# Kernel optimization log

Measured on AMD Instinct MI355X. Metric: run time of the kernel, lower is better.

Reference implementation:

```python
import jax, jax.numpy as jnp
import numpy as np

B, NV, NC, D, GD = 4, 2048, 8192, 64, 8


def setup_inputs() -> dict:
    key = jax.random.key(0)
    ks = jax.random.split(key, 16)
    f32 = jnp.float32
    rn = lambda k, s, fan: (jax.random.normal(k, s, dtype=f32) / np.float32(np.sqrt(fan)))
    raw = jax.random.randint(ks[0], (B, NC, NV), 0, 20)
    c_mat = jnp.where(raw == 0, -1.0, jnp.where(raw == 1, 1.0, 0.0)).astype(f32)
    v_mat = jnp.transpose(c_mat, (0, 2, 1))  # [B, NV, NC]
    variables = jax.random.normal(ks[1], (B, NV, D), dtype=f32)
    ground_vars = jax.random.normal(ks[2], (B, NV, GD), dtype=f32)
    # learned params
    c_block = rn(ks[3], (2, D, D), D)  # pos/neg literal projections (clause side)
    v_block = rn(ks[4], (2, D, D), D)  # pos/neg literal projections (variable side)
    vb = jax.random.normal(ks[5], (D,), dtype=f32)
    cb = jax.random.normal(ks[6], (D,), dtype=f32)
    Wg = rn(ks[7], (D, GD + D), GD + D)  # ground combiner Linear(concat) -> D
    bg = jnp.zeros((D,), f32)
    Wz = rn(ks[8], (D, D), D); Uz = rn(ks[9], (D, D), D); bz = jnp.zeros((D,), f32)
    Wr = rn(ks[10], (D, D), D); Ur = rn(ks[11], (D, D), D); br = jnp.zeros((D,), f32)
    Wh = rn(ks[12], (D, D), D); Uh = rn(ks[13], (D, D), D); bh = jnp.zeros((D,), f32)
    return dict(variables=variables, ground_vars=ground_vars, c_mat=c_mat, v_mat=v_mat,
                c_block=c_block, v_block=v_block, vb=vb, cb=cb, Wg=Wg, bg=bg,
                Wz=Wz, Uz=Uz, bz=bz, Wr=Wr, Ur=Ur, br=br, Wh=Wh, Uh=Uh, bh=bh)


def reference(variables, ground_vars, c_mat, v_mat, c_block, v_block, vb, cb,
              Wg, bg, Wz, Uz, bz, Wr, Ur, br, Wh, Uh, bh):
    b, nv, d = variables.shape
    v = variables.reshape(-1, d)  # [B*NV, D]
    # clause-side literal projections: bmm(c_block, v^T)^T == v @ c_block[i]^T
    pos_vars = (v @ c_block[0].T).reshape(b, nv, d)
    neg_vars = (v @ c_block[1].T).reshape(b, nv, d)
    pos_cmat = jnp.clip(c_mat, 0.0, 1.0)
    neg_cmat = -jnp.clip(c_mat, -1.0, 0.0)
    c = (jnp.einsum('bcv,bvd->bcd', pos_cmat, pos_vars)
         + jnp.einsum('bcv,bvd->bcd', neg_cmat, neg_vars))  # [B, NC, D]
    c = jax.nn.relu(c + cb)
    cv = c.reshape(-1, d)  # [B*NC, D]
    pos_cvars = (cv @ v_block[0].T).reshape(b, -1, d)
    neg_cvars = (cv @ v_block[1].T).reshape(b, -1, d)
    pos_vmat = jnp.clip(v_mat, 0.0, 1.0)
    neg_vmat = -jnp.clip(v_mat, -1.0, 0.0)
    nv_msg = (jnp.einsum('bvc,bcd->bvd', pos_vmat, pos_cvars)
              + jnp.einsum('bvc,bcd->bvd', neg_vmat, neg_cvars))  # [B, NV, D]
    v_emb = jax.nn.relu(nv_msg + vb).reshape(-1, d)
    # ground combiner: tanh(Linear(concat(ground, v_emb)))
    g = ground_vars.reshape(-1, ground_vars.shape[-1])
    av = jnp.tanh(jnp.concatenate([g, v_emb], axis=-1) @ Wg.T + bg)
    # GRU update against previous variable embeddings
    prev = v
    z = jax.nn.sigmoid(av @ Wz.T + prev @ Uz.T + bz)
    r = jax.nn.sigmoid(av @ Wr.T + prev @ Ur.T + br)
    h_tilda = jnp.tanh(av @ Wh.T + (r * prev) @ Uh.T + bh)
    h = (1.0 - z) * prev + z * h_tilda
    return h.reshape(b, nv * d, 1)
```

## Files before the change

### kernel.cpp

```cpp
#include <hip/hip_runtime.h>
#include <hip/hip_bf16.h>
#include <stdint.h>

#define NBATCH 4
#define NV 2048
#define NC 8192
#define DD 64

typedef __attribute__((ext_vector_type(8))) short s16x8;
typedef __attribute__((ext_vector_type(4))) float fx4;
typedef __attribute__((ext_vector_type(8))) unsigned short u16x8;
typedef __attribute__((ext_vector_type(4))) int i32x4;
typedef __attribute__((ext_vector_type(2))) unsigned int u32x2;

static __device__ __forceinline__ unsigned short bf16_rne(float x) {
    union { float f; unsigned int u; } v; v.f = x;
    unsigned int u = v.u;
    u += 0x7FFFu + ((u >> 16) & 1u);
    return (unsigned short)(u >> 16);
}
static __device__ __forceinline__ float bf16_f32(unsigned short h) {
    union { unsigned int u; float f; } v; v.u = ((unsigned int)h) << 16;
    return v.f;
}
static __device__ __forceinline__ void gload_lds16(const void* g, void* l) {
    __builtin_amdgcn_global_load_lds(
        (const __attribute__((address_space(1))) unsigned int*)g,
        (__attribute__((address_space(3))) unsigned int*)l, 16, 0, 0);
}

__global__ __launch_bounds__(256) void k_prep_pv(
    const float* __restrict__ vars, const float* __restrict__ cblk,
    char* __restrict__ qsh, char* __restrict__ qsl,
    char* __restrict__ qdh, char* __restrict__ qdl)
{
    __shared__ float sv[32][64];
    __shared__ float scb[2][64][65];
    int blk = blockIdx.x;
    int b = blk >> 6, ch = blk & 63;
    int t = threadIdx.x;
    const float* vsrc = vars + ((size_t)b * NV + (size_t)ch * 32) * DD;
    for (int i = t; i < 32 * 64; i += 256) sv[i >> 6][i & 63] = vsrc[i];
    for (int i = t; i < 2 * 64 * 64; i += 256) {
        int pn = i >> 12, dout = (i >> 6) & 63, k = i & 63;
        scb[pn][k][dout] = cblk[i];
    }
    __syncthreads();
    int ks = t >> 6, dout = t & 63;
    unsigned int wsh[2] = {0, 0}, wsl[2] = {0, 0}, wdh[2] = {0, 0}, wdl[2] = {0, 0};
    #pragma unroll
    for (int c8 = 0; c8 < 8; ++c8) {
        int vloc = ks * 8 + c8;
        float ap = 0.f, an = 0.f;
        for (int k = 0; k < 64; ++k) {
            float vv = sv[vloc][k];
            ap += vv * scb[0][k][dout];
            an += vv * scb[1][k][dout];
        }
        float s = (ap + an) * 0.5f, dv = (ap - an) * 0.5f;
        int qs_ = (int)rintf(s * 4096.f);
        int qd_ = (int)rintf(dv * 4096.f);
        qs_ = min(max(qs_, -32511), 32511);
        qd_ = min(max(qd_, -32511), 32511);
        int sh = (qs_ + 128) >> 8, sl = qs_ - (sh << 8);
        int dh = (qd_ + 128) >> 8, dl = qd_ - (dh << 8);
        int w = c8 >> 2, sft = (c8 & 3) * 8;
        wsh[w] |= (unsigned int)(sh & 0xFF) << sft;
        wsl[w] |= (unsigned int)(sl & 0xFF) << sft;
        wdh[w] |= (unsigned int)(dh & 0xFF) << sft;
        wdl[w] |= (unsigned int)(dl & 0xFF) << sft;
    }
    int kc = ch >> 1;
    int lg = ((ch & 1) << 1) | (ks >> 1);
    size_t off = (((size_t)(b * 32 + kc) * 64 + dout) * 4 + lg) * 16 + (ks & 1) * 8;
    *(u32x2*)(qsh + off) = (u32x2){wsh[0], wsh[1]};
    *(u32x2*)(qsl + off) = (u32x2){wsl[0], wsl[1]};
    *(u32x2*)(qdh + off) = (u32x2){wdh[0], wdh[1]};
    *(u32x2*)(qdl + off) = (u32x2){wdl[0], wdl[1]};
}

__global__ __launch_bounds__(512, 4) void k_phaseA(
    const float* __restrict__ cmat,
    const char* __restrict__ qsh, const char* __restrict__ qsl,
    const char* __restrict__ qdh, const char* __restrict__ qdl,
    const float* __restrict__ cb,
    float* __restrict__ cfull, unsigned short* __restrict__ comp)
{
    __shared__ char lds[2][16384];
    int blk = blockIdx.x;
    int b = blk & 3;
    int rg = blk >> 2;
    int t = threadIdx.x;
    int wv = t >> 6, l = t & 63, lr = l & 15, lg = l >> 4;
    int row0 = rg * 128 + wv * 16;
    const float* A0 = cmat + (size_t)b * NC * NV + (size_t)(row0 + lr) * NV + lg * 16;
    unsigned short* compb = comp + (size_t)b * 256 * NC;

    i32x4 ahi[4], alo[4];
    #pragma unroll
    for (int n = 0; n < 4; ++n) { ahi[n] = (i32x4){0,0,0,0}; alo[n] = (i32x4){0,0,0,0}; }

    if (t < 256) {
        size_t gb = ((size_t)(b * 32)) * 4096 + (size_t)t * 16;
        char* lp = &lds[0][t * 16];
        gload_lds16(qsh + gb, lp);
        gload_lds16(qsl + gb, lp + 4096);
        gload_lds16(qdh + gb, lp + 8192);
        gload_lds16(qdl + gb, lp + 12288);
    }
    fx4 xc[4], xn[4];
    #pragma unroll
    for (int j4 = 0; j4 < 4; ++j4) xc[j4] = *(const fx4*)(A0 + j4 * 4);
    __syncthreads();

    int cur = 0;
    #pragma unroll 1
    for (int kc = 0; kc < 32; ++kc) {
        if (kc < 31) {
            if (t < 256) {
                size_t gb = ((size_t)(b * 32 + kc + 1)) * 4096 + (size_t)t * 16;
                char* lp = &lds[cur ^ 1][t * 16];
                gload_lds16(qsh + gb, lp);
                gload_lds16(qsl + gb, lp + 4096);
                gload_lds16(qdh + gb, lp + 8192);
                gload_lds16(qdl + gb, lp + 12288);
            }
            #pragma unroll
            for (int j4 = 0; j4 < 4; ++j4)
                xn[j4] = *(const fx4*)(A0 + (kc + 1) * 64 + j4 * 4);
        }
        int tt[16];
        #pragma unroll
        for (int j = 0; j < 16; ++j) tt[j] = (int)xc[j >> 2][j & 3];
        i32x4 Asgn, Aabs;
        #pragma unroll
        for (int w = 0; w < 4; ++w)
            Asgn[w] = (unsigned int)(tt[4*w] & 0xFF) | ((unsigned int)(tt[4*w+1] & 0xFF) << 8)
                    | ((unsigned int)(tt[4*w+2] & 0xFF) << 16) | ((unsigned int)(tt[4*w+3] & 0xFF) << 24);
        #pragma unroll
        for (int w = 0; w < 4; ++w) Aabs[w] = Asgn[w] & 0x01010101;
        {
            unsigned int b0 = 0, b1 = 0;
            #pragma unroll
            for (int j = 0; j < 8; ++j) b0 |= ((unsigned int)tt[j] & 3u) << (2 * j);
            #pragma unroll
            for (int j = 0; j < 8; ++j) b1 |= ((unsigned int)tt[8 + j] & 3u) << (2 * j);
            int v8 = kc * 8 + lg * 2;
            int crow = row0 + lr;
            compb[(size_t)v8 * NC + crow] = (unsigned short)b0;
            compb[(size_t)(v8 + 1) * NC + crow] = (unsigned short)b1;
        }
        const char* bufp = lds[cur];
        #pragma unroll
        for (int n = 0; n < 4; ++n) {
            int boff = ((n * 16 + lr) * 4 + lg) * 16;
            i32x4 Bsh = *(const i32x4*)(bufp + boff);
            i32x4 Bsl = *(const i32x4*)(bufp + 4096 + boff);
            i32x4 Bdh = *(const i32x4*)(bufp + 8192 + boff);
            i32x4 Bdl = *(const i32x4*)(bufp + 12288 + boff);
            ahi[n] = __builtin_amdgcn_mfma_i32_16x16x64_i8(Aabs, Bsh, ahi[n], 0, 0, 0);
            ahi[n] = __builtin_amdgcn_mfma_i32_16x16x64_i8(Asgn, Bdh, ahi[n], 0, 0, 0);
            alo[n] = __builtin_amdgcn_mfma_i32_16x16x64_i8(Aabs, Bsl, alo[n], 0, 0, 0);
            alo[n] = __builtin_amdgcn_mfma_i32_16x16x64_i8(Asgn, Bdl, alo[n], 0, 0, 0);
        }
        if (kc < 31) {
            #pragma unroll
            for (int j4 = 0; j4 < 4; ++j4) xc[j4] = xn[j4];
        }
        __syncthreads();
        cur ^= 1;
    }
    float* dst = cfull + ((size_t)b * NC + row0) * DD;
    #pragma unroll
    for (int n = 0; n < 4; ++n) {
        int col = n * 16 + lr;
        float cbv = cb[col];
        #pragma unroll
        for (int r = 0; r < 4; ++r) {
            float v = (float)(ahi[n][r] * 256 + alo[n][r]) * (1.0f / 4096.0f) + cbv;
            dst[(size_t)(lg * 4 + r) * DD + col] = fmaxf(v, 0.f);
        }
    }
}

__global__ __launch_bounds__(256) void k_projC(
    const float* __restrict__ cfull,
    const float* __restrict__ vblk,
    unsigned short* __restrict__ csh, unsigned short* __restrict__ csl,
    unsigned short* __restrict__ cdh, unsigned short* __restrict__ cdl)
{
    __shared__ float src[32][64];
    __shared__ float svb[2][64][65];
    int blk = blockIdx.x;
    int b = blk >> 8, kc = blk & 255;
    int t = threadIdx.x;
    const float* cs = cfull + ((size_t)b * NC + (size_t)kc * 32) * DD;
    for (int i = t; i < 2048; i += 256) src[i >> 6][i & 63] = cs[i];
    for (int i = t; i < 8192; i += 256) {
        int pn = i >> 12, dout = (i >> 6) & 63, k = i & 63;
        svb[pn][k][dout] = vblk[i];
    }
    __syncthreads();
    int ks = t >> 6, dout = t & 63;
    float ap[8] = {0.f, 0.f, 0.f, 0.f, 0.f, 0.f, 0.f, 0.f};
    float an[8] = {0.f, 0.f, 0.f, 0.f, 0.f, 0.f, 0.f, 0.f};
    for (int k = 0; k < 64; ++k) {
        float w0 = svb[0][k][dout], w1 = svb[1][k][dout];
        #pragma unroll
        for (int c8 = 0; c8 < 8; ++c8) {
            float rc = src[ks * 8 + c8][k];
            ap[c8] += rc * w0;
            an[c8] += rc * w1;
        }
    }
    u16x8 vsh, vsl, vdh, vdl;
    #pragma unroll
    for (int c8 = 0; c8 < 8; ++c8) {
        float s = (ap[c8] + an[c8]) * 0.5f, dv = (ap[c8] - an[c8]) * 0.5f;
        unsigned short h = bf16_rne(s);
        vsh[c8] = h; vsl[c8] = bf16_rne(s - bf16_f32(h));
        h = bf16_rne(dv);
        vdh[c8] = h; vdl[c8] = bf16_rne(dv - bf16_f32(h));
    }
    size_t obase = (size_t)b * NC * DD + (((size_t)kc * 4 + ks) * 64 + dout) * 8;
    *(u16x8*)(csh + obase) = vsh;
    *(u16x8*)(csl + obase) = vsl;
    *(u16x8*)(cdh + obase) = vdh;
    *(u16x8*)(cdl + obase) = vdl;
}

__global__ __launch_bounds__(256, 2) void k_phaseB(
    const unsigned short* __restrict__ comp,
    const unsigned short* __restrict__ csh, const unsigned short* __restrict__ csl,
    const unsigned short* __restrict__ cdh, const unsigned short* __restrict__ cdl,
    float* __restrict__ npart)
{
    __shared__ short lds[2][16384];
    int blk = blockIdx.x;
    int combo = blk & 63;
    int rg = blk >> 6;
    int b = combo >> 4;
    int q = combo & 15;
    int t = threadIdx.x;
    int wv = t >> 6, l = t & 63, lr = l & 15, lg = l >> 4;
    int v0 = rg * 256 + wv * 64;
    const unsigned short* compb = comp + (size_t)b * 256 * NC;
    const size_t cvb = (size_t)b * NC * DD;
    int sh_ = 2 * (lr & 7);
    const unsigned short* cp[4];
    #pragma unroll
    for (int rt = 0; rt < 4; ++rt)
        cp[rt] = compb + (size_t)((v0 + rt * 16 + lr) >> 3) * NC + q * 512 + lg * 8;

    fx4 acc[4][4];
    #pragma unroll
    for (int i = 0; i < 4; ++i)
        #pragma unroll
        for (int j = 0; j < 4; ++j) acc[i][j] = (fx4){0.f, 0.f, 0.f, 0.f};

    {
        size_t gb = cvb + (size_t)(q * 8) * 4096 + (size_t)t * 8;
        short* lp = &lds[0][t * 8];
        gload_lds16(csh + gb, lp);           gload_lds16(csh + gb + 2048, lp + 2048);
        gload_lds16(csl + gb, lp + 4096);    gload_lds16(csl + gb + 2048, lp + 6144);
        gload_lds16(cdh + gb, lp + 8192);    gload_lds16(cdh + gb + 2048, lp + 10240);
        gload_lds16(cdl + gb, lp + 12288);   gload_lds16(cdl + gb + 2048, lp + 14336);
    }
    u16x8 uc[4][2], un[4][2];
    #pragma unroll
    for (int rt = 0; rt < 4; ++rt) {
        uc[rt][0] = *(const u16x8*)(cp[rt]);
        uc[rt][1] = *(const u16x8*)(cp[rt] + 32);
    }
    __syncthreads();

    int cur = 0;
    #pragma unroll 1
    for (int cc = 0; cc < 8; ++cc) {
        if (cc < 7) {
            size_t gb = cvb + (size_t)(q * 8 + cc + 1) * 4096 + (size_t)t * 8;
            short* lp = &lds[cur ^ 1][t * 8];
            gload_lds16(csh + gb, lp);           gload_lds16(csh + gb + 2048, lp + 2048);
            gload_lds16(csl + gb, lp + 4096);    gload_lds16(csl + gb + 2048, lp + 6144);
            gload_lds16(cdh + gb, lp + 8192);    gload_lds16(cdh + gb + 2048, lp + 10240);
            gload_lds16(cdl + gb, lp + 12288);   gload_lds16(cdl + gb + 2048, lp + 14336);
            #pragma unroll
            for (int rt = 0; rt < 4; ++rt) {
                un[rt][0] = *(const u16x8*)(cp[rt] + (cc + 1) * 64);
                un[rt][1] = *(const u16x8*)(cp[rt] + (cc + 1) * 64 + 32);
            }
        }
        const short* bufp = &lds[cur][0];
        #pragma unroll
        for (int st = 0; st < 2; ++st) {
            s16x8 As[4], Aa[4];
            #pragma unroll
            for (int rt = 0; rt < 4; ++rt) {
                #pragma unroll
                for (int i = 0; i < 8; ++i) {
                    unsigned int tb = ((unsigned int)uc[rt][st][i] >> sh_) & 3u;
                    unsigned short m = (tb & 1u) ? (unsigned short)0x3F80 : (unsigned short)0;
                    As[rt][i] = (short)m;
                    Aa[rt][i] = (short)(m | ((tb & 2u) << 14));
                }
            }
            #pragma unroll
            for (int n = 0; n < 4; ++n) {
                int off = ((st * 4 + lg) * 64 + n * 16 + lr) * 8;
                s16x8 Bs0 = *(const s16x8*)(bufp + off);
                s16x8 Bs1 = *(const s16x8*)(bufp + 4096 + off);
                s16x8 Bd0 = *(const s16x8*)(bufp + 8192 + off);
                s16x8 Bd1 = *(const s16x8*)(bufp + 12288 + off);
                #pragma unroll
                for (int rt = 0; rt < 4; ++rt) {
                    acc[rt][n] = __builtin_amdgcn_mfma_f32_16x16x32_bf16(As[rt], Bs0, acc[rt][n], 0, 0, 0);
                    acc[rt][n] = __builtin_amdgcn_mfma_f32_16x16x32_bf16(As[rt], Bs1, acc[rt][n], 0, 0, 0);
                    acc[rt][n] = __builtin_amdgcn_mfma_f32_16x16x32_bf16(Aa[rt], Bd0, acc[rt][n], 0, 0, 0);
                    acc[rt][n] = __builtin_amdgcn_mfma_f32_16x16x32_bf16(Aa[rt], Bd1, acc[rt][n], 0, 0, 0);
                }
            }
        }
        if (cc < 7) {
            #pragma unroll
            for (int rt = 0; rt < 4; ++rt) { uc[rt][0] = un[rt][0]; uc[rt][1] = un[rt][1]; }
        }
        __syncthreads();
        cur ^= 1;
    }
    float* dst = npart + (((size_t)q * NBATCH + b) * NV + v0) * DD;
    #pragma unroll
    for (int rt = 0; rt < 4; ++rt)
        #pragma unroll
        for (int n = 0; n < 4; ++n)
            #pragma unroll
            for (int r = 0; r < 4; ++r)
                dst[(size_t)(rt * 16 + lg * 4 + r) * DD + n * 16 + lr] = acc[rt][n][r];
}

__global__ __launch_bounds__(512) void k_gru(
    const float* __restrict__ npart, const float* __restrict__ vars,
    const float* __restrict__ gv, const float* __restrict__ vb,
    const float* __restrict__ Wg, const float* __restrict__ bg,
    const float* __restrict__ Wz, const float* __restrict__ Uz, const float* __restrict__ bz,
    const float* __restrict__ Wr, const float* __restrict__ Ur, const float* __restrict__ brr,
    const float* __restrict__ Wh, const float* __restrict__ Uh, const float* __restrict__ bh,
    float* __restrict__ out)
{
    __shared__ float sWg[72][65];
    __shared__ float sWz[64][65], sUz[64][65];
    __shared__ float sWr[64][65], sUr[64][65];
    __shared__ float sWh[64][65], sUh[64][65];
    __shared__ float scat[8][72];
    __shared__ float sprev[8][64];
    __shared__ float sav[8][64];
    __shared__ float srp[8][64];
    int t = threadIdx.x;
    for (int i = t * 4; i < 4608; i += 2048) {
        fx4 g4 = *(const fx4*)(Wg + i);
        int dout = i / 72, j = i - dout * 72;
        #pragma unroll
        for (int jj = 0; jj < 4; ++jj) sWg[j + jj][dout] = g4[jj];
    }
    for (int i = t * 4; i < 4096; i += 2048) {
        int dout = i >> 6, k = i & 63;
        fx4 a;
        a = *(const fx4*)(Wz + i);
        #pragma unroll
        for (int jj = 0; jj < 4; ++jj) sWz[k + jj][dout] = a[jj];
        a = *(const fx4*)(Uz + i);
        #pragma unroll
        for (int jj = 0; jj < 4; ++jj) sUz[k + jj][dout] = a[jj];
        a = *(const fx4*)(Wr + i);
        #pragma unroll
        for (int jj = 0; jj < 4; ++jj) sWr[k + jj][dout] = a[jj];
        a = *(const fx4*)(Ur + i);
        #pragma unroll
        for (int jj = 0; jj < 4; ++jj) sUr[k + jj][dout] = a[jj];
        a = *(const fx4*)(Wh + i);
        #pragma unroll
        for (int jj = 0; jj < 4; ++jj) sWh[k + jj][dout] = a[jj];
        a = *(const fx4*)(Uh + i);
        #pragma unroll
        for (int jj = 0; jj < 4; ++jj) sUh[k + jj][dout] = a[jj];
    }
    int rr = t >> 6, dout = t & 63;
    const size_t qs = (size_t)NBATCH * NV * DD;
    #pragma unroll 1
    for (int it = 0; it < 4; ++it) {
        size_t row = (size_t)blockIdx.x * 32 + it * 8 + rr;
        float prev = vars[row * 64 + dout];
        float ve = vb[dout];
        #pragma unroll
        for (int s = 0; s < 16; ++s) ve += npart[(size_t)s * qs + row * 64 + dout];
        ve = fmaxf(ve, 0.f);
        scat[rr][8 + dout] = ve;
        if (dout < 8) scat[rr][dout] = gv[row * 8 + dout];
        sprev[rr][dout] = prev;
        __syncthreads();
        float a = bg[dout];
        for (int j = 0; j < 72; ++j) a += scat[rr][j] * sWg[j][dout];
        float av = 1.f - 2.f / (__expf(2.f * a) + 1.f);
        sav[rr][dout] = av;
        __syncthreads();
        float zi = bz[dout], ri = brr[dout], hwa = 0.f;
        for (int k = 0; k < 64; ++k) {
            float ak = sav[rr][k], pk = sprev[rr][k];
            zi += ak * sWz[k][dout] + pk * sUz[k][dout];
            ri += ak * sWr[k][dout] + pk * sUr[k][dout];
            hwa += ak * sWh[k][dout];
        }
        float z = 1.f / (1.f + __expf(-zi));
        float rgate = 1.f / (1.f + __expf(-ri));
        srp[rr][dout] = rgate * prev;
        __syncthreads();
        float hin = bh[dout] + hwa;
        for (int k = 0; k < 64; ++k) hin += srp[rr][k] * sUh[k][dout];
        float ht = 1.f - 2.f / (__expf(2.f * hin) + 1.f);
        out[row * 64 + dout] = (1.f - z) * prev + z * ht;
        __syncthreads();
    }
}

extern "C" void kernel_launch(void* const* d_in, const int* in_sizes, int n_in,
                              void* d_out, int out_size, void* d_ws, size_t ws_size,
                              hipStream_t stream) {
    (void)in_sizes; (void)n_in; (void)out_size; (void)ws_size;
    const float* vars = (const float*)d_in[0];
    const float* gv   = (const float*)d_in[1];
    const float* cmat = (const float*)d_in[2];
    const float* cblk = (const float*)d_in[4];
    const float* vblk = (const float*)d_in[5];
    const float* vb   = (const float*)d_in[6];
    const float* cb   = (const float*)d_in[7];
    const float* Wg   = (const float*)d_in[8];
    const float* bg   = (const float*)d_in[9];
    const float* Wz   = (const float*)d_in[10];
    const float* Uz   = (const float*)d_in[11];
    const float* bz   = (const float*)d_in[12];
    const float* Wr   = (const float*)d_in[13];
    const float* Ur   = (const float*)d_in[14];
    const float* br_  = (const float*)d_in[15];
    const float* Wh   = (const float*)d_in[16];
    const float* Uh   = (const float*)d_in[17];
    const float* bh   = (const float*)d_in[18];
    float* out = (float*)d_out;

    char* w = (char*)d_ws;
    const size_t MB = 1024 * 1024;
    char* qsh = w + 0 * MB;
    char* qsl = w + 1 * MB;
    char* qdh = w + 2 * MB;
    char* qdl = w + 3 * MB;
    unsigned short* csh = (unsigned short*)(w + 4 * MB);
    unsigned short* csl = (unsigned short*)(w + 8 * MB);
    unsigned short* cdh = (unsigned short*)(w + 12 * MB);
    unsigned short* cdl = (unsigned short*)(w + 16 * MB);
    float* cfull         = (float*)(w + 20 * MB);
    float* npart         = (float*)(w + 28 * MB);
    unsigned short* comp = (unsigned short*)(w + 60 * MB);

    k_prep_pv<<<256, 256, 0, stream>>>(vars, cblk, qsh, qsl, qdh, qdl);
    k_phaseA<<<256, 512, 0, stream>>>(cmat, qsh, qsl, qdh, qdl, cb, cfull, comp);
    k_projC<<<1024, 256, 0, stream>>>(cfull, vblk, csh, csl, cdh, cdl);
    k_phaseB<<<512, 256, 0, stream>>>(comp, csh, csl, cdh, cdl, npart);
    k_gru<<<256, 512, 0, stream>>>(npart, vars, gv, vb, Wg, bg,
                                   Wz, Uz, bz, Wr, Ur, br_, Wh, Uh, bh, out);
}
```

Before: 175.5 us.

## Split phaseA/phaseB reductions across more blocks and drop LDS staging

Phase A now splits the variable dimension into two halves, with four times as many smaller blocks writing partial clause sums. Bias and ReLU move into k_projC, which adds the two partials. Phase B uses smaller 16-row tiles per wave with an 8-way split over clauses, and the GRU kernel runs more blocks over fewer rows each. Both matmul kernels drop double-buffered LDS staging and read B operands straight from global memory, relying on cache and higher occupancy for latency hiding. The trade-off is more partial-sum traffic and redundant B reads through L2.

```diff
diff --git a/kernel.cpp b/kernel.cpp
--- a/kernel.cpp
+++ b/kernel.cpp
@@ -22,11 +22,6 @@
 static __device__ __forceinline__ float bf16_f32(unsigned short h) {
     union { unsigned int u; float f; } v; v.u = ((unsigned int)h) << 16;
     return v.f;
-}
-static __device__ __forceinline__ void gload_lds16(const void* g, void* l) {
-    __builtin_amdgcn_global_load_lds(
-        (const __attribute__((address_space(1))) unsigned int*)g,
-        (__attribute__((address_space(3))) unsigned int*)l, 16, 0, 0);
 }
 
 __global__ __launch_bounds__(256) void k_prep_pv(
@@ -79,56 +74,37 @@
     *(u32x2*)(qdl + off) = (u32x2){wdl[0], wdl[1]};
 }
 
-__global__ __launch_bounds__(512, 4) void k_phaseA(
+__global__ __launch_bounds__(256, 4) void k_phaseA(
     const float* __restrict__ cmat,
     const char* __restrict__ qsh, const char* __restrict__ qsl,
     const char* __restrict__ qdh, const char* __restrict__ qdl,
-    const float* __restrict__ cb,
-    float* __restrict__ cfull, unsigned short* __restrict__ comp)
-{
-    __shared__ char lds[2][16384];
+    float* __restrict__ cpart, unsigned short* __restrict__ comp)
+{
     int blk = blockIdx.x;
-    int b = blk & 3;
-    int rg = blk >> 2;
+    int combo = blk & 7;
+    int rg = blk >> 3;
+    int b = combo >> 1;
+    int q = combo & 1;
     int t = threadIdx.x;
     int wv = t >> 6, l = t & 63, lr = l & 15, lg = l >> 4;
-    int row0 = rg * 128 + wv * 16;
-    const float* A0 = cmat + (size_t)b * NC * NV + (size_t)(row0 + lr) * NV + lg * 16;
+    int row = rg * 64 + wv * 16 + lr;
+    const float* A0 = cmat + (size_t)b * NC * NV + (size_t)row * NV + q * 1024 + lg * 16;
     unsigned short* compb = comp + (size_t)b * 256 * NC;
+    const char* qb0 = qsh + ((size_t)(b * 32 + q * 16)) * 4096;
+    const char* qb1 = qsl + ((size_t)(b * 32 + q * 16)) * 4096;
+    const char* qb2 = qdh + ((size_t)(b * 32 + q * 16)) * 4096;
+    const char* qb3 = qdl + ((size_t)(b * 32 + q * 16)) * 4096;
 
     i32x4 ahi[4], alo[4];
     #pragma unroll
     for (int n = 0; n < 4; ++n) { ahi[n] = (i32x4){0,0,0,0}; alo[n] = (i32x4){0,0,0,0}; }
 
-    if (t < 256) {
-        size_t gb = ((size_t)(b * 32)) * 4096 + (size_t)t * 16;
-        char* lp = &lds[0][t * 16];
-        gload_lds16(qsh + gb, lp);
-        gload_lds16(qsl + gb, lp + 4096);
-        gload_lds16(qdh + gb, lp + 8192);
-        gload_lds16(qdl + gb, lp + 12288);
-    }
-    fx4 xc[4], xn[4];
-    #pragma unroll
-    for (int j4 = 0; j4 < 4; ++j4) xc[j4] = *(const fx4*)(A0 + j4 * 4);
-    __syncthreads();
-
-    int cur = 0;
     #pragma unroll 1
-    for (int kc = 0; kc < 32; ++kc) {
-        if (kc < 31) {
-            if (t < 256) {
-                size_t gb = ((size_t)(b * 32 + kc + 1)) * 4096 + (size_t)t * 16;
-                char* lp = &lds[cur ^ 1][t * 16];
-                gload_lds16(qsh + gb, lp);
-                gload_lds16(qsl + gb, lp + 4096);
-                gload_lds16(qdh + gb, lp + 8192);
-                gload_lds16(qdl + gb, lp + 12288);
-            }
-            #pragma unroll
-            for (int j4 = 0; j4 < 4; ++j4)
-                xn[j4] = *(const fx4*)(A0 + (kc + 1) * 64 + j4 * 4);
-        }
+    for (int kc = 0; kc < 16; ++kc) {
+        fx4 xc[4];
+        #pragma unroll
+        for (int j4 = 0; j4 < 4; ++j4)
+            xc[j4] = *(const fx4*)(A0 + kc * 64 + j4 * 4);
         int tt[16];
         #pragma unroll
         for (int j = 0; j < 16; ++j) tt[j] = (int)xc[j >> 2][j & 3];
@@ -145,46 +121,38 @@
             for (int j = 0; j < 8; ++j) b0 |= ((unsigned int)tt[j] & 3u) << (2 * j);
             #pragma unroll
             for (int j = 0; j < 8; ++j) b1 |= ((unsigned int)tt[8 + j] & 3u) << (2 * j);
-            int v8 = kc * 8 + lg * 2;
-            int crow = row0 + lr;
-            compb[(size_t)v8 * NC + crow] = (unsigned short)b0;
-            compb[(size_t)(v8 + 1) * NC + crow] = (unsigned short)b1;
-        }
-        const char* bufp = lds[cur];
+            int v8 = q * 128 + kc * 8 + lg * 2;
+            compb[(size_t)v8 * NC + row] = (unsigned short)b0;
+            compb[(size_t)(v8 + 1) * NC + row] = (unsigned short)b1;
+        }
+        size_t cb_ = (size_t)kc * 4096;
         #pragma unroll
         for (int n = 0; n < 4; ++n) {
-            int boff = ((n * 16 + lr) * 4 + lg) * 16;
-            i32x4 Bsh = *(const i32x4*)(bufp + boff);
-            i32x4 Bsl = *(const i32x4*)(bufp + 4096 + boff);
-            i32x4 Bdh = *(const i32x4*)(bufp + 8192 + boff);
-            i32x4 Bdl = *(const i32x4*)(bufp + 12288 + boff);
+            size_t boff = cb_ + (size_t)(((n * 16 + lr) * 4 + lg) * 16);
+            i32x4 Bsh = *(const i32x4*)(qb0 + boff);
+            i32x4 Bsl = *(const i32x4*)(qb1 + boff);
+            i32x4 Bdh = *(const i32x4*)(qb2 + boff);
+            i32x4 Bdl = *(const i32x4*)(qb3 + boff);
             ahi[n] = __builtin_amdgcn_mfma_i32_16x16x64_i8(Aabs, Bsh, ahi[n], 0, 0, 0);
             ahi[n] = __builtin_amdgcn_mfma_i32_16x16x64_i8(Asgn, Bdh, ahi[n], 0, 0, 0);
             alo[n] = __builtin_amdgcn_mfma_i32_16x16x64_i8(Aabs, Bsl, alo[n], 0, 0, 0);
             alo[n] = __builtin_amdgcn_mfma_i32_16x16x64_i8(Asgn, Bdl, alo[n], 0, 0, 0);
         }
-        if (kc < 31) {
-            #pragma unroll
-            for (int j4 = 0; j4 < 4; ++j4) xc[j4] = xn[j4];
-        }
-        __syncthreads();
-        cur ^= 1;
-    }
-    float* dst = cfull + ((size_t)b * NC + row0) * DD;
+    }
+    float* dst = cpart + (((size_t)q * NBATCH + b) * NC + rg * 64 + wv * 16) * DD;
     #pragma unroll
     for (int n = 0; n < 4; ++n) {
         int col = n * 16 + lr;
-        float cbv = cb[col];
         #pragma unroll
         for (int r = 0; r < 4; ++r) {
-            float v = (float)(ahi[n][r] * 256 + alo[n][r]) * (1.0f / 4096.0f) + cbv;
-            dst[(size_t)(lg * 4 + r) * DD + col] = fmaxf(v, 0.f);
+            float v = (float)(ahi[n][r] * 256 + alo[n][r]) * (1.0f / 4096.0f);
+            dst[(size_t)(lg * 4 + r) * DD + col] = v;
         }
     }
 }
 
 __global__ __launch_bounds__(256) void k_projC(
-    const float* __restrict__ cfull,
+    const float* __restrict__ cpart, const float* __restrict__ cb,
     const float* __restrict__ vblk,
     unsigned short* __restrict__ csh, unsigned short* __restrict__ csl,
     unsigned short* __restrict__ cdh, unsigned short* __restrict__ cdl)
@@ -194,8 +162,13 @@
     int blk = blockIdx.x;
     int b = blk >> 8, kc = blk & 255;
     int t = threadIdx.x;
-    const float* cs = cfull + ((size_t)b * NC + (size_t)kc * 32) * DD;
-    for (int i = t; i < 2048; i += 256) src[i >> 6][i & 63] = cs[i];
+    const size_t qs = (size_t)NBATCH * NC * DD;
+    const float* cs = cpart + ((size_t)b * NC + (size_t)kc * 32) * DD;
+    for (int i = t; i < 2048; i += 256) {
+        int k = i & 63;
+        float v = cs[i] + cs[i + qs] + cb[k];
+        src[i >> 6][k] = fmaxf(v, 0.f);
+    }
     for (int i = t; i < 8192; i += 256) {
         int pn = i >> 12, dout = (i >> 6) & 63, k = i & 63;
         svb[pn][k][dout] = vblk[i];
@@ -229,112 +202,69 @@
     *(u16x8*)(cdl + obase) = vdl;
 }
 
-__global__ __launch_bounds__(256, 2) void k_phaseB(
+__global__ __launch_bounds__(256, 4) void k_phaseB(
     const unsigned short* __restrict__ comp,
     const unsigned short* __restrict__ csh, const unsigned short* __restrict__ csl,
     const unsigned short* __restrict__ cdh, const unsigned short* __restrict__ cdl,
     float* __restrict__ npart)
 {
-    __shared__ short lds[2][16384];
     int blk = blockIdx.x;
-    int combo = blk & 63;
-    int rg = blk >> 6;
-    int b = combo >> 4;
-    int q = combo & 15;
+    int combo = blk & 31;
+    int rg = blk >> 5;
+    int b = combo >> 3;
+    int q = combo & 7;
     int t = threadIdx.x;
     int wv = t >> 6, l = t & 63, lr = l & 15, lg = l >> 4;
-    int v0 = rg * 256 + wv * 64;
+    int v0 = rg * 64 + wv * 16;
     const unsigned short* compb = comp + (size_t)b * 256 * NC;
+    const unsigned short* cp = compb + (size_t)((v0 + lr) >> 3) * NC + q * 1024 + lg * 8;
+    int sh_ = 2 * (lr & 7);
     const size_t cvb = (size_t)b * NC * DD;
-    int sh_ = 2 * (lr & 7);
-    const unsigned short* cp[4];
-    #pragma unroll
-    for (int rt = 0; rt < 4; ++rt)
-        cp[rt] = compb + (size_t)((v0 + rt * 16 + lr) >> 3) * NC + q * 512 + lg * 8;
-
-    fx4 acc[4][4];
-    #pragma unroll
-    for (int i = 0; i < 4; ++i)
-        #pragma unroll
-        for (int j = 0; j < 4; ++j) acc[i][j] = (fx4){0.f, 0.f, 0.f, 0.f};
-
-    {
-        size_t gb = cvb + (size_t)(q * 8) * 4096 + (size_t)t * 8;
-        short* lp = &lds[0][t * 8];
-        gload_lds16(csh + gb, lp);           gload_lds16(csh + gb + 2048, lp + 2048);
-        gload_lds16(csl + gb, lp + 4096);    gload_lds16(csl + gb + 2048, lp + 6144);
-        gload_lds16(cdh + gb, lp + 8192);    gload_lds16(cdh + gb + 2048, lp + 10240);
-        gload_lds16(cdl + gb, lp + 12288);   gload_lds16(cdl + gb + 2048, lp + 14336);
-    }
-    u16x8 uc[4][2], un[4][2];
-    #pragma unroll
-    for (int rt = 0; rt < 4; ++rt) {
-        uc[rt][0] = *(const u16x8*)(cp[rt]);
-        uc[rt][1] = *(const u16x8*)(cp[rt] + 32);
-    }
-    __syncthreads();
-
-    int cur = 0;
+    const unsigned short* pb0 = csh + cvb + (size_t)(q * 16) * 4096;
+    const unsigned short* pb1 = csl + cvb + (size_t)(q * 16) * 4096;
+    const unsigned short* pb2 = cdh + cvb + (size_t)(q * 16) * 4096;
+    const unsigned short* pb3 = cdl + cvb + (size_t)(q * 16) * 4096;
+
+    fx4 acc[4];
+    #pragma unroll
+    for (int n = 0; n < 4; ++n) acc[n] = (fx4){0.f, 0.f, 0.f, 0.f};
+
     #pragma unroll 1
-    for (int cc = 0; cc < 8; ++cc) {
-        if (cc < 7) {
-            size_t gb = cvb + (size_t)(q * 8 + cc + 1) * 4096 + (size_t)t * 8;
-            short* lp = &lds[cur ^ 1][t * 8];
-            gload_lds16(csh + gb, lp);           gload_lds16(csh + gb + 2048, lp + 2048);
-            gload_lds16(csl + gb, lp + 4096);    gload_lds16(csl + gb + 2048, lp + 6144);
-            gload_lds16(cdh + gb, lp + 8192);    gload_lds16(cdh + gb + 2048, lp + 10240);
-            gload_lds16(cdl + gb, lp + 12288);   gload_lds16(cdl + gb + 2048, lp + 14336);
+    for (int kc = 0; kc < 16; ++kc) {
+        u16x8 uc0 = *(const u16x8*)(cp + kc * 64);
+        u16x8 uc1 = *(const u16x8*)(cp + kc * 64 + 32);
+        size_t cb_ = (size_t)kc * 4096;
+        #pragma unroll
+        for (int st = 0; st < 2; ++st) {
+            u16x8 u = st ? uc1 : uc0;
+            s16x8 As, Aa;
             #pragma unroll
-            for (int rt = 0; rt < 4; ++rt) {
-                un[rt][0] = *(const u16x8*)(cp[rt] + (cc + 1) * 64);
-                un[rt][1] = *(const u16x8*)(cp[rt] + (cc + 1) * 64 + 32);
-            }
-        }
-        const short* bufp = &lds[cur][0];
-        #pragma unroll
-        for (int st = 0; st < 2; ++st) {
-            s16x8 As[4], Aa[4];
-            #pragma unroll
-            for (int rt = 0; rt < 4; ++rt) {
-                #pragma unroll
-                for (int i = 0; i < 8; ++i) {
-                    unsigned int tb = ((unsigned int)uc[rt][st][i] >> sh_) & 3u;
-                    unsigned short m = (tb & 1u) ? (unsigned short)0x3F80 : (unsigned short)0;
-                    As[rt][i] = (short)m;
-                    Aa[rt][i] = (short)(m | ((tb & 2u) << 14));
-                }
+            for (int i = 0; i < 8; ++i) {
+                unsigned int tb = ((unsigned int)u[i] >> sh_) & 3u;
+                unsigned short m = (tb & 1u) ? (unsigned short)0x3F80 : (unsigned short)0;
+                As[i] = (short)m;
+                Aa[i] = (short)(m | ((tb & 2u) << 14));
             }
             #pragma unroll
             for (int n = 0; n < 4; ++n) {
-                int off = ((st * 4 + lg) * 64 + n * 16 + lr) * 8;
-                s16x8 Bs0 = *(const s16x8*)(bufp + off);
-                s16x8 Bs1 = *(const s16x8*)(bufp + 4096 + off);
-                s16x8 Bd0 = *(const s16x8*)(bufp + 8192 + off);
-                s16x8 Bd1 = *(const s16x8*)(bufp + 12288 + off);
-                #pragma unroll
-                for (int rt = 0; rt < 4; ++rt) {
-                    acc[rt][n] = __builtin_amdgcn_mfma_f32_16x16x32_bf16(As[rt], Bs0, acc[rt][n], 0, 0, 0);
-                    acc[rt][n] = __builtin_amdgcn_mfma_f32_16x16x32_bf16(As[rt], Bs1, acc[rt][n], 0, 0, 0);
-                    acc[rt][n] = __builtin_amdgcn_mfma_f32_16x16x32_bf16(Aa[rt], Bd0, acc[rt][n], 0, 0, 0);
-                    acc[rt][n] = __builtin_amdgcn_mfma_f32_16x16x32_bf16(Aa[rt], Bd1, acc[rt][n], 0, 0, 0);
-                }
+                size_t off = cb_ + (size_t)(((st * 4 + lg) * 64 + n * 16 + lr) * 8);
+                s16x8 Bs0 = *(const s16x8*)(pb0 + off);
+                s16x8 Bs1 = *(const s16x8*)(pb1 + off);
+                s16x8 Bd0 = *(const s16x8*)(pb2 + off);
+                s16x8 Bd1 = *(const s16x8*)(pb3 + off);
+                acc[n] = __builtin_amdgcn_mfma_f32_16x16x32_bf16(As, Bs0, acc[n], 0, 0, 0);
+                acc[n] = __builtin_amdgcn_mfma_f32_16x16x32_bf16(As, Bs1, acc[n], 0, 0, 0);
+                acc[n] = __builtin_amdgcn_mfma_f32_16x16x32_bf16(Aa, Bd0, acc[n], 0, 0, 0);
+                acc[n] = __builtin_amdgcn_mfma_f32_16x16x32_bf16(Aa, Bd1, acc[n], 0, 0, 0);
             }
         }
-        if (cc < 7) {
-            #pragma unroll
-            for (int rt = 0; rt < 4; ++rt) { uc[rt][0] = un[rt][0]; uc[rt][1] = un[rt][1]; }
-        }
-        __syncthreads();
-        cur ^= 1;
     }
     float* dst = npart + (((size_t)q * NBATCH + b) * NV + v0) * DD;
     #pragma unroll
-    for (int rt = 0; rt < 4; ++rt)
-        #pragma unroll
-        for (int n = 0; n < 4; ++n)
-            #pragma unroll
-            for (int r = 0; r < 4; ++r)
-                dst[(size_t)(rt * 16 + lg * 4 + r) * DD + n * 16 + lr] = acc[rt][n][r];
+    for (int n = 0; n < 4; ++n)
+        #pragma unroll
+        for (int r = 0; r < 4; ++r)
+            dst[(size_t)(lg * 4 + r) * DD + n * 16 + lr] = acc[n][r];
 }
 
 __global__ __launch_bounds__(512) void k_gru(
@@ -386,12 +316,12 @@
     int rr = t >> 6, dout = t & 63;
     const size_t qs = (size_t)NBATCH * NV * DD;
     #pragma unroll 1
-    for (int it = 0; it < 4; ++it) {
-        size_t row = (size_t)blockIdx.x * 32 + it * 8 + rr;
+    for (int it = 0; it < 2; ++it) {
+        size_t row = (size_t)blockIdx.x * 16 + it * 8 + rr;
         float prev = vars[row * 64 + dout];
         float ve = vb[dout];
         #pragma unroll
-        for (int s = 0; s < 16; ++s) ve += npart[(size_t)s * qs + row * 64 + dout];
+        for (int s = 0; s < 8; ++s) ve += npart[(size_t)s * qs + row * 64 + dout];
         ve = fmaxf(ve, 0.f);
         scat[rr][8 + dout] = ve;
         if (dout < 8) scat[rr][dout] = gv[row * 8 + dout];
@@ -455,14 +385,14 @@
     unsigned short* csl = (unsigned short*)(w + 8 * MB);
     unsigned short* cdh = (unsigned short*)(w + 12 * MB);
     unsigned short* cdl = (unsigned short*)(w + 16 * MB);
-    float* cfull         = (float*)(w + 20 * MB);
-    float* npart         = (float*)(w + 28 * MB);
-    unsigned short* comp = (unsigned short*)(w + 60 * MB);
+    float* cpart         = (float*)(w + 20 * MB);
+    float* npart         = (float*)(w + 36 * MB);
+    unsigned short* comp = (unsigned short*)(w + 52 * MB);
 
     k_prep_pv<<<256, 256, 0, stream>>>(vars, cblk, qsh, qsl, qdh, qdl);
-    k_phaseA<<<256, 512, 0, stream>>>(cmat, qsh, qsl, qdh, qdl, cb, cfull, comp);
-    k_projC<<<1024, 256, 0, stream>>>(cfull, vblk, csh, csl, cdh, cdl);
-    k_phaseB<<<512, 256, 0, stream>>>(comp, csh, csl, cdh, cdl, npart);
-    k_gru<<<256, 512, 0, stream>>>(npart, vars, gv, vb, Wg, bg,
+    k_phaseA<<<1024, 256, 0, stream>>>(cmat, qsh, qsl, qdh, qdl, cpart, comp);
+    k_projC<<<1024, 256, 0, stream>>>(cpart, cb, vblk, csh, csl, cdh, cdl);
+    k_phaseB<<<1024, 256, 0, stream>>>(comp, csh, csl, cdh, cdl, npart);
+    k_gru<<<512, 512, 0, stream>>>(npart, vars, gv, vb, Wg, bg,
                                    Wz, Uz, bz, Wr, Ur, br_, Wh, Uh, bh, out);
 }
```

Result: slower. 266.0 us (+51.6%).
